# Kernel optimization log

Hardware: AMD Instinct MI355X
Metric: run time of the kernel (lower is better)

## Reference

```python
import jax, jax.numpy as jnp
import numpy as np

B, N, D, H = 8, 512, 128, 128


def setup_inputs() -> dict:
    key = jax.random.key(0)
    ks = jax.random.split(key, 8)
    F0 = jax.random.normal(ks[0], (B, N, D), dtype=jnp.float32)
    mask = jax.random.randint(ks[1], (B, N), 0, 2).astype(bool)
    # Linear params, torch convention: y = x @ W.T + b
    W1 = jax.random.normal(ks[2], (H, 3 * D), dtype=jnp.float32) / np.sqrt(3 * D)
    b1 = jax.random.normal(ks[3], (H,), dtype=jnp.float32) * 0.01
    W2 = jax.random.normal(ks[4], (64, H), dtype=jnp.float32) / np.sqrt(H)
    b2 = jax.random.normal(ks[5], (64,), dtype=jnp.float32) * 0.01
    W3 = jax.random.normal(ks[6], (1, 64), dtype=jnp.float32) / np.sqrt(64)
    b3 = jax.random.normal(ks[7], (1,), dtype=jnp.float32) * 0.01
    return {"F0": F0, "mask": mask, "W1": W1, "b1": b1, "W2": W2, "b2": b2, "W3": W3, "b3": b3}


def reference(F0, mask, W1, b1, W2, b2, W3, b3):
    d = F0.shape[-1]
    # Decompose Linear(3D,H) over cat([fi, fj, fi-fj]):
    #   W1 @ [fi; fj; fi-fj] = fi @ (Wa+Wc).T + fj @ (Wb-Wc).T
    Wa, Wb, Wc = W1[:, :d], W1[:, d:2 * d], W1[:, 2 * d:]
    pi = F0 @ (Wa + Wc).T            # [B,N,H]
    pj = F0 @ (Wb - Wc).T            # [B,N,H]
    h1 = jax.nn.relu(pi[:, :, None, :] + pj[:, None, :, :] + b1)   # [B,N,N,H]
    h2 = jax.nn.relu(jnp.einsum('bijh,oh->bijo', h1, W2) + b2)     # [B,N,N,64]
    logit = jnp.einsum('bijo,o->bij', h2, W3[0]) + b3[0]           # [B,N,N]
    pair_mask = mask[:, :, None] & mask[:, None, :]
    neg_fill = jnp.float32(-1e9)
    logit = jnp.where(pair_mask, logit, neg_fill)
    return jax.nn.sigmoid(logit)
```

## Files before the change

### kernel.cpp

```cpp
#include <hip/hip_runtime.h>

#define B 8
#define N 512
#define D 128
#define H 128
#define IC 16
#define JT 64
#define NF 1024

typedef __attribute__((ext_vector_type(8))) _Float16 f16x8;
typedef __attribute__((ext_vector_type(2))) __fp16 fp16x2;
typedef __attribute__((ext_vector_type(4))) float f32x4;

union F8 { uint4 u; f16x8 f; };
union H8 { f16x8 f; fp16x2 p[4]; };

__device__ __host__ inline int w2perm(int g, int m) {
    return ((g >> 1) << 5) + ((m >> 2) << 3) + ((g & 1) << 2) + (m & 3);
}

__global__ __launch_bounds__(256) void prep_kernel(
        const float* __restrict__ W1, const float* __restrict__ W2,
        const float* __restrict__ b1, const float* __restrict__ b2,
        const float* __restrict__ W3, const int* __restrict__ mask,
        float4* __restrict__ out4,
        _Float16* __restrict__ Wpq, _Float16* __restrict__ W2h,
        float* __restrict__ b1e, float* __restrict__ b2p,
        _Float16* __restrict__ w3h,
        int* __restrict__ idx, int* __restrict__ cnt) {
    int blk = blockIdx.x;
    int tid = threadIdx.x;
    if (blk < NF) {
        int base = blk * 512 + tid;
        out4[base]       = float4{0.f, 0.f, 0.f, 0.f};
        out4[base + 256] = float4{0.f, 0.f, 0.f, 0.f};
    } else if (blk < NF + 64) {
        int t = (blk - NF) * 256 + tid;
        if (t < H * D) {
            int h = t >> 7, k = t & 127;
            float wa = W1[h * 384 + k];
            float wb = W1[h * 384 + 128 + k];
            float wc = W1[h * 384 + 256 + k];
            Wpq[h * 128 + k]         = (_Float16)(wa + wc);
            Wpq[(128 + h) * 128 + k] = (_Float16)(wb - wc);
        }
        if (t < 64 * H) {
            int on = t >> 7, k = t & 127;
            int pi = w2perm(on >> 4, on & 15);
            W2h[t] = (_Float16)W2[pi * 128 + k];
        }
        if (t < 256) b1e[t] = (t < 128) ? b1[t] : 0.f;
        if (t < 64) {
            int pi = w2perm(t >> 4, t & 15);
            b2p[t] = b2[pi];
            w3h[t] = (_Float16)W3[t];
        }
    } else {
        int b = blk - NF - 64;
        int lane = tid;
        if (lane >= 64) return;
        const int* m = mask + b * N;
        int base = 0;
        for (int ch = 0; ch < N / 64; ++ch) {
            int v = m[ch * 64 + lane];
            unsigned long long bal = __ballot(v != 0);
            int pos = base + __popcll(bal & ((1ull << lane) - 1ull));
            if (v) idx[b * N + pos] = ch * 64 + lane;
            base += __popcll(bal);
        }
        if (lane == 0) cnt[b] = base;
    }
}

__global__ __launch_bounds__(64) void pq_mfma_kernel(const float* __restrict__ F0,
                                                     const _Float16* __restrict__ Wpq,
                                                     const float* __restrict__ b1e,
                                                     _Float16* __restrict__ PQ) {
    int r0 = blockIdx.x * 16;
    int cb = blockIdx.y * 64;
    int lane = threadIdx.x;
    int lp = lane & 15, lg = lane >> 4;

    __shared__ _Float16 T[16][64];

    f16x8 af[4];
    const float* fr = F0 + (size_t)(r0 + lp) * D;
#pragma unroll
    for (int ks = 0; ks < 4; ++ks) {
        float4 a0 = *(const float4*)(fr + ks * 32 + lg * 8);
        float4 a1 = *(const float4*)(fr + ks * 32 + lg * 8 + 4);
        f16x8 v;
        v[0] = (_Float16)a0.x; v[1] = (_Float16)a0.y;
        v[2] = (_Float16)a0.z; v[3] = (_Float16)a0.w;
        v[4] = (_Float16)a1.x; v[5] = (_Float16)a1.y;
        v[6] = (_Float16)a1.z; v[7] = (_Float16)a1.w;
        af[ks] = v;
    }

#pragma unroll
    for (int ct = 0; ct < 4; ++ct) {
        int col = cb + ct * 16 + lp;
        const _Float16* wrow = Wpq + (size_t)col * 128;
        f32x4 acc = 0.f;
#pragma unroll
        for (int ks = 0; ks < 4; ++ks) {
            f16x8 bf = *(const f16x8*)(wrow + ks * 32 + lg * 8);
            acc = __builtin_amdgcn_mfma_f32_16x16x32_f16(af[ks], bf, acc, 0, 0, 0);
        }
        float b1v = b1e[col];
#pragma unroll
        for (int e = 0; e < 4; ++e)
            T[lg * 4 + e][ct * 16 + lp] = (_Float16)(acc[e] + b1v);
    }
    __syncthreads();

    int r  = lane >> 2;
    int c4 = (lane & 3) * 16;
    uint4 v0 = *(const uint4*)&T[r][c4];
    uint4 v1 = *(const uint4*)&T[r][c4 + 8];
    _Float16* dst = PQ + (size_t)(r0 + r) * 256 + cb + c4;
    *(uint4*)dst       = v0;
    *(uint4*)(dst + 8) = v1;
}

__global__ __launch_bounds__(256, 3) void pair_mfma_kernel(
        const _Float16* __restrict__ PQ,
        const _Float16* __restrict__ W2h,
        const float* __restrict__ b2p, const _Float16* __restrict__ w3h,
        const float* __restrict__ b3v,
        const int* __restrict__ idx, const int* __restrict__ cnt,
        float* __restrict__ out) {
    int t = blockIdx.x;
    int b = -1, local = 0, nv = 0, acc = 0;
#pragma unroll
    for (int k = 0; k < B; ++k) {
        int c   = cnt[k];
        int nTi = (c + IC - 1) / IC;
        int nTj = (c + JT - 1) / JT;
        int tl  = nTi * nTj;
        if (b < 0 && t < acc + tl) { b = k; local = t - acc; nv = c; }
        acc += tl;
    }
    if (b < 0) return;
    int nTj = (nv + JT - 1) / JT;
    int i0  = (local / nTj) * IC;
    int j0  = (local % nTj) * JT;

    int tid  = threadIdx.x;
    int lane = tid & 63;
    int w    = tid >> 6;
    int lg   = lane >> 4;
    int lp   = lane & 15;

    __shared__ uint4 W2s[64][16];
    __shared__ uint4 Pl[IC][16];
    __shared__ int   iI[IC];

    {
        const uint4* W2v = (const uint4*)W2h;
#pragma unroll
        for (int q = 0; q < 4; ++q) {
            int m = tid + q * 256;
            int r = m >> 4, u = m & 15;
            W2s[r][u ^ (r & 15)] = W2v[m];
        }
    }
    {
        int r = tid >> 4, c = tid & 15;
        int ir = i0 + r;
        int ivr = idx[b * N + (ir < nv ? ir : nv - 1)];
        if (c == 0) iI[r] = ivr;
        Pl[r][c] = *(const uint4*)(PQ + ((size_t)(b * N) + ivr) * 256 + c * 8);
    }
    __syncthreads();

    const uint4* pw0 = &W2s[lp][(0 * 4 + lg) ^ lp];
    const uint4* pw1 = &W2s[lp][(1 * 4 + lg) ^ lp];
    const uint4* pw2 = &W2s[lp][(2 * 4 + lg) ^ lp];
    const uint4* pw3 = &W2s[lp][(3 * 4 + lg) ^ lp];

    int jj   = j0 + w * 16 + lp;
    bool jok = jj < nv;
    int jidx = idx[b * N + (jok ? jj : nv - 1)];
    F8 qf[4];
    {
        const _Float16* qrow = PQ + ((size_t)(b * N) + jidx) * 256 + 128;
#pragma unroll
        for (int c = 0; c < 4; ++c)
            qf[c].u = *(const uint4*)(qrow + c * 32 + lg * 8);
    }

    f32x4 b2v[4];
#pragma unroll
    for (int g = 0; g < 4; ++g)
        b2v[g] = *(const f32x4*)(b2p + g * 16 + lg * 4);
    f16x8 w3f0 = *(const f16x8*)(w3h + lg * 8);
    f16x8 w3f1 = *(const f16x8*)(w3h + 32 + lg * 8);
    float b3s = b3v[0];
    const f32x4 z4 = 0.f;
    const f16x8 zh = (f16x8)(_Float16)0;

    size_t outbase = ((size_t)(b * N)) * N;

#define CSTEP2(IIA, IIB, C, PW)                                                \
    {                                                                          \
        F8 phA; phA.u = Pl[IIA][(C) * 4 + lg];                                 \
        F8 phB; phB.u = Pl[IIB][(C) * 4 + lg];                                 \
        f16x8 hvA = __builtin_elementwise_max(phA.f + qf[C].f, zh);            \
        f16x8 hvB = __builtin_elementwise_max(phB.f + qf[C].f, zh);            \
        F8 a0, a1, a2, a3;                                                     \
        a0.u = PW[0 * 256]; a1.u = PW[1 * 256];                                \
        a2.u = PW[2 * 256]; a3.u = PW[3 * 256];                                \
        accA[0] = __builtin_amdgcn_mfma_f32_16x16x32_f16(a0.f, hvA, accA[0], 0, 0, 0); \
        accB[0] = __builtin_amdgcn_mfma_f32_16x16x32_f16(a0.f, hvB, accB[0], 0, 0, 0); \
        accA[1] = __builtin_amdgcn_mfma_f32_16x16x32_f16(a1.f, hvA, accA[1], 0, 0, 0); \
        accB[1] = __builtin_amdgcn_mfma_f32_16x16x32_f16(a1.f, hvB, accB[1], 0, 0, 0); \
        accA[2] = __builtin_amdgcn_mfma_f32_16x16x32_f16(a2.f, hvA, accA[2], 0, 0, 0); \
        accB[2] = __builtin_amdgcn_mfma_f32_16x16x32_f16(a2.f, hvB, accB[2], 0, 0, 0); \
        accA[3] = __builtin_amdgcn_mfma_f32_16x16x32_f16(a3.f, hvA, accA[3], 0, 0, 0); \
        accB[3] = __builtin_amdgcn_mfma_f32_16x16x32_f16(a3.f, hvB, accB[3], 0, 0, 0); \
    }

#define EPI(ACC, II)                                                           \
    {                                                                          \
        f32x4 t0 = __builtin_elementwise_max(ACC[0] + b2v[0], z4);             \
        f32x4 t1 = __builtin_elementwise_max(ACC[1] + b2v[1], z4);             \
        f32x4 t2 = __builtin_elementwise_max(ACC[2] + b2v[2], z4);             \
        f32x4 t3 = __builtin_elementwise_max(ACC[3] + b2v[3], z4);             \
        H8 h0, h1;                                                             \
        h0.p[0] = __builtin_amdgcn_cvt_pkrtz(t0[0], t0[1]);                    \
        h0.p[1] = __builtin_amdgcn_cvt_pkrtz(t0[2], t0[3]);                    \
        h0.p[2] = __builtin_amdgcn_cvt_pkrtz(t1[0], t1[1]);                    \
        h0.p[3] = __builtin_amdgcn_cvt_pkrtz(t1[2], t1[3]);                    \
        h1.p[0] = __builtin_amdgcn_cvt_pkrtz(t2[0], t2[1]);                    \
        h1.p[1] = __builtin_amdgcn_cvt_pkrtz(t2[2], t2[3]);                    \
        h1.p[2] = __builtin_amdgcn_cvt_pkrtz(t3[0], t3[1]);                    \
        h1.p[3] = __builtin_amdgcn_cvt_pkrtz(t3[2], t3[3]);                    \
        f32x4 rac0 = {b3s, b3s, b3s, b3s};                                     \
        f32x4 rac1 = 0.f;                                                      \
        rac0 = __builtin_amdgcn_mfma_f32_16x16x32_f16(w3f0, h0.f, rac0, 0, 0, 0); \
        rac1 = __builtin_amdgcn_mfma_f32_16x16x32_f16(w3f1, h1.f, rac1, 0, 0, 0); \
        float logit = rac0[0] + rac1[0];                                       \
        float val = 1.f / (1.f + __expf(-logit));                              \
        if (lane < 16 && jok && (i0 + (II)) < nv)                              \
            out[outbase + (size_t)iI[II] * N + jidx] = val;                    \
    }

    f32x4 accA[4], accB[4];
#pragma unroll 1
    for (int ii = 0; ii < IC; ii += 2) {
#pragma unroll
        for (int g = 0; g < 4; ++g) { accA[g] = 0.f; accB[g] = 0.f; }
        CSTEP2(ii, ii + 1, 0, pw0)
        CSTEP2(ii, ii + 1, 1, pw1)
        CSTEP2(ii, ii + 1, 2, pw2)
        CSTEP2(ii, ii + 1, 3, pw3)
        EPI(accA, ii)
        EPI(accB, ii + 1)
    }

#undef CSTEP2
#undef EPI
}

extern "C" void kernel_launch(void* const* d_in, const int* in_sizes, int n_in,
                              void* d_out, int out_size, void* d_ws, size_t ws_size,
                              hipStream_t stream) {
    const float* F0  = (const float*)d_in[0];
    const int*   msk = (const int*)  d_in[1];
    const float* W1  = (const float*)d_in[2];
    const float* b1  = (const float*)d_in[3];
    const float* W2  = (const float*)d_in[4];
    const float* b2  = (const float*)d_in[5];
    const float* W3  = (const float*)d_in[6];
    const float* b3  = (const float*)d_in[7];
    float* out = (float*)d_out;

    char* ws = (char*)d_ws;
    _Float16* PQ  = (_Float16*)ws;
    _Float16* Wpq = (_Float16*)(ws + (2u << 20));
    _Float16* W2h = (_Float16*)(ws + (2u << 20) + (64u << 10));
    float*    b1e = (float*)   (ws + (2u << 20) + (80u << 10));
    float*    b2p = (float*)   (ws + (2u << 20) + (81u << 10));
    _Float16* w3h = (_Float16*)(ws + (2u << 20) + (82u << 10));
    int*      idx = (int*)     (ws + (2u << 20) + (84u << 10));
    int*      cnt = (int*)     (ws + (2u << 20) + (100u << 10));

    prep_kernel<<<NF + 64 + 8, 256, 0, stream>>>(W1, W2, b1, b2, W3, msk,
                                                 (float4*)out, Wpq, W2h, b1e, b2p,
                                                 w3h, idx, cnt);
    pq_mfma_kernel<<<dim3(B * N / 16, 4), 64, 0, stream>>>(F0, Wpq, b1e, PQ);

    int maxTiles = B * ((N + IC - 1) / IC) * ((N + JT - 1) / JT);
    pair_mfma_kernel<<<maxTiles, 256, 0, stream>>>(
        PQ, W2h, b2p, w3h, b3, idx, cnt, out);
}
```

Measured before the change: 32.40 us.

## Halve i-tile, move epilogue constants to LDS to raise occupancy

Cuts the i-tile from 16 to 8 rows per block and raises the launch-bounds minimum from 3 to 4 blocks per CU. The b2 and w3 epilogue constants now sit in shared memory and are re-read through volatile pointers on every epilogue, so they no longer hold registers. The goal is lower register pressure and more resident waves to hide latency. In exchange there are more blocks, each W2 tile staged into LDS serves fewer rows, and every epilogue does extra LDS reads.

```diff
diff --git a/kernel.cpp b/kernel.cpp
--- a/kernel.cpp
+++ b/kernel.cpp
@@ -4,7 +4,7 @@
 #define N 512
 #define D 128
 #define H 128
-#define IC 16
+#define IC 8
 #define JT 64
 #define NF 1024
 
@@ -14,6 +14,7 @@
 
 union F8 { uint4 u; f16x8 f; };
 union H8 { f16x8 f; fp16x2 p[4]; };
+union U16 { unsigned long long u[2]; f32x4 f; f16x8 h; };
 
 __device__ __host__ inline int w2perm(int g, int m) {
     return ((g >> 1) << 5) + ((m >> 2) << 3) + ((g & 1) << 2) + (m & 3);
@@ -123,7 +124,7 @@
     *(uint4*)(dst + 8) = v1;
 }
 
-__global__ __launch_bounds__(256, 3) void pair_mfma_kernel(
+__global__ __launch_bounds__(256, 4) void pair_mfma_kernel(
         const _Float16* __restrict__ PQ,
         const _Float16* __restrict__ W2h,
         const float* __restrict__ b2p, const _Float16* __restrict__ w3h,
@@ -155,6 +156,8 @@
     __shared__ uint4 W2s[64][16];
     __shared__ uint4 Pl[IC][16];
     __shared__ int   iI[IC];
+    __shared__ float b2s[64];
+    __shared__ _Float16 w3s[64];
 
     {
         const uint4* W2v = (const uint4*)W2h;
@@ -165,12 +168,16 @@
             W2s[r][u ^ (r & 15)] = W2v[m];
         }
     }
-    {
+    if (tid < IC * 16) {
         int r = tid >> 4, c = tid & 15;
         int ir = i0 + r;
         int ivr = idx[b * N + (ir < nv ? ir : nv - 1)];
         if (c == 0) iI[r] = ivr;
         Pl[r][c] = *(const uint4*)(PQ + ((size_t)(b * N) + ivr) * 256 + c * 8);
+    }
+    if (tid < 64) {
+        b2s[tid] = b2p[tid];
+        w3s[tid] = w3h[tid];
     }
     __syncthreads();
 
@@ -190,15 +197,14 @@
             qf[c].u = *(const uint4*)(qrow + c * 32 + lg * 8);
     }
 
-    f32x4 b2v[4];
-#pragma unroll
-    for (int g = 0; g < 4; ++g)
-        b2v[g] = *(const f32x4*)(b2p + g * 16 + lg * 4);
-    f16x8 w3f0 = *(const f16x8*)(w3h + lg * 8);
-    f16x8 w3f1 = *(const f16x8*)(w3h + 32 + lg * 8);
     float b3s = b3v[0];
     const f32x4 z4 = 0.f;
     const f16x8 zh = (f16x8)(_Float16)0;
+
+    const volatile unsigned long long* b2q =
+        (const volatile unsigned long long*)b2s;
+    const volatile unsigned long long* w3q =
+        (const volatile unsigned long long*)w3s;
 
     size_t outbase = ((size_t)(b * N)) * N;
 
@@ -223,10 +229,17 @@
 
 #define EPI(ACC, II)                                                           \
     {                                                                          \
-        f32x4 t0 = __builtin_elementwise_max(ACC[0] + b2v[0], z4);             \
-        f32x4 t1 = __builtin_elementwise_max(ACC[1] + b2v[1], z4);             \
-        f32x4 t2 = __builtin_elementwise_max(ACC[2] + b2v[2], z4);             \
-        f32x4 t3 = __builtin_elementwise_max(ACC[3] + b2v[3], z4);             \
+        U16 bb0, bb1, bb2, bb3, ww0, ww1;                                      \
+        bb0.u[0] = b2q[(0 * 4 + lg) * 2]; bb0.u[1] = b2q[(0 * 4 + lg) * 2 + 1];\
+        bb1.u[0] = b2q[(1 * 4 + lg) * 2]; bb1.u[1] = b2q[(1 * 4 + lg) * 2 + 1];\
+        bb2.u[0] = b2q[(2 * 4 + lg) * 2]; bb2.u[1] = b2q[(2 * 4 + lg) * 2 + 1];\
+        bb3.u[0] = b2q[(3 * 4 + lg) * 2]; bb3.u[1] = b2q[(3 * 4 + lg) * 2 + 1];\
+        ww0.u[0] = w3q[lg * 2];     ww0.u[1] = w3q[lg * 2 + 1];                \
+        ww1.u[0] = w3q[8 + lg * 2]; ww1.u[1] = w3q[8 + lg * 2 + 1];            \
+        f32x4 t0 = __builtin_elementwise_max(ACC[0] + bb0.f, z4);              \
+        f32x4 t1 = __builtin_elementwise_max(ACC[1] + bb1.f, z4);              \
+        f32x4 t2 = __builtin_elementwise_max(ACC[2] + bb2.f, z4);              \
+        f32x4 t3 = __builtin_elementwise_max(ACC[3] + bb3.f, z4);              \
         H8 h0, h1;                                                             \
         h0.p[0] = __builtin_amdgcn_cvt_pkrtz(t0[0], t0[1]);                    \
         h0.p[1] = __builtin_amdgcn_cvt_pkrtz(t0[2], t0[3]);                    \
@@ -238,8 +251,8 @@
         h1.p[3] = __builtin_amdgcn_cvt_pkrtz(t3[2], t3[3]);                    \
         f32x4 rac0 = {b3s, b3s, b3s, b3s};                                     \
         f32x4 rac1 = 0.f;                                                      \
-        rac0 = __builtin_amdgcn_mfma_f32_16x16x32_f16(w3f0, h0.f, rac0, 0, 0, 0); \
-        rac1 = __builtin_amdgcn_mfma_f32_16x16x32_f16(w3f1, h1.f, rac1, 0, 0, 0); \
+        rac0 = __builtin_amdgcn_mfma_f32_16x16x32_f16(ww0.h, h0.f, rac0, 0, 0, 0); \
+        rac1 = __builtin_amdgcn_mfma_f32_16x16x32_f16(ww1.h, h1.f, rac1, 0, 0, 0); \
         float logit = rac0[0] + rac1[0];                                       \
         float val = 1.f / (1.f + __expf(-logit));                              \
         if (lane < 16 && jok && (i0 + (II)) < nv)                              \
```

Result: slower. 124.9 us (+285.5%).
